# Kernel tuning notes

Hardware: AMD Instinct MI355X
Metric: run time of the kernel (lower is better)

## Reference

```python
import jax, jax.numpy as jnp
import numpy as np
from functools import partial

N = 50000
IN_C, HID_C, OUT_C = 256, 128, 64
E = 800000


def gcn_norm(src, dst, n_nodes):
    # PyG gcn_norm with unit edge weights: deg from target index, D^-1/2 A D^-1/2
    ones = jnp.ones(src.shape[0], dtype=jnp.float32)
    deg = jax.ops.segment_sum(ones, dst, num_segments=n_nodes)
    dinv = jnp.where(deg > 0, jax.lax.rsqrt(deg), 0.0)
    return dinv[src] * dinv[dst]


def gcn_conv(x, src, dst, norm, W, b):
    h = x @ W                              # [N, out] dense GEMM first (PyG order)
    msg = h[src] * norm[:, None]           # gather + scale  [E', out]
    out = jax.ops.segment_sum(msg, dst, num_segments=x.shape[0])
    return out + b


def setup_inputs() -> dict:
    key = jax.random.key(0)
    ks = jax.random.split(key, 6)
    x = jax.random.normal(ks[0], (N, IN_C), dtype=jnp.float32)
    edge_index = jax.random.randint(ks[1], (2, E), 0, N, dtype=jnp.int32)
    # Glorot-ish init for weights
    W1 = jax.random.normal(ks[2], (IN_C, HID_C), dtype=jnp.float32) / np.sqrt(IN_C)
    b1 = jnp.zeros((HID_C,), dtype=jnp.float32)
    W2 = jax.random.normal(ks[3], (HID_C, OUT_C), dtype=jnp.float32) / np.sqrt(HID_C)
    b2 = jnp.zeros((OUT_C,), dtype=jnp.float32)
    return {"x": x, "edge_index": edge_index, "W1": W1, "b1": b1, "W2": W2, "b2": b2}


def reference(x, edge_index, W1, b1, W2, b2):
    # eval mode: dropout is identity
    n = x.shape[0]
    loop = jnp.arange(n, dtype=edge_index.dtype)
    src = jnp.concatenate([edge_index[0], loop])   # add self loops (static E+N)
    dst = jnp.concatenate([edge_index[1], loop])
    norm = gcn_norm(src, dst, n)
    h = jax.nn.relu(gcn_conv(x, src, dst, norm, W1, b1))
    return gcn_conv(h, src, dst, norm, W2, b2)
```

## Files before the change

### kernel.cpp

```cpp
#include <hip/hip_runtime.h>


#define TPB 256
#define NBKT 196
#define P1_BLKS 98
#define PB_CAP 96
#define EB_CAP 4608
#define CSR_CAP 6400
#define P1_EPB 8192

typedef __bf16 bf16x8 __attribute__((ext_vector_type(8)));
typedef __bf16 bf16x4 __attribute__((ext_vector_type(4)));
typedef __bf16 bf16x2 __attribute__((ext_vector_type(2)));
typedef float f32x4 __attribute__((ext_vector_type(4)));

__device__ __forceinline__ float bflo(unsigned u) { return __uint_as_float(u << 16); }
__device__ __forceinline__ float bfhi(unsigned u) { return __uint_as_float(u & 0xffff0000u); }

__device__ __forceinline__ void gemm1_body(int bid, int tid, const float* __restrict__ x,
                                           const float* __restrict__ W1,
                                           __bf16* __restrict__ outp, int M) {
    int wave = tid >> 6, lane = tid & 63;
    int col = lane & 15, q = lane >> 4;
    long rb = (long)bid * 128 + wave * 32;
    long r0 = rb + col, r1 = rb + 16 + col;
    long r0c = (r0 < M) ? r0 : (M - 1);
    long r1c = (r1 < M) ? r1 : (M - 1);

    f32x4 acc[8][2];
#pragma unroll
    for (int o = 0; o < 8; o++) {
        acc[o][0] = (f32x4){0.f, 0.f, 0.f, 0.f};
        acc[o][1] = (f32x4){0.f, 0.f, 0.f, 0.f};
    }

#pragma unroll
    for (int ks = 0; ks < 8; ks++) {
        int k0 = ks * 32 + q * 8;
        const float* A0 = x + r0c * 256 + k0;
        const float* A1 = x + r1c * 256 + k0;
        float4 f0a = *(const float4*)A0;
        float4 f0b = *(const float4*)(A0 + 4);
        float4 f1a = *(const float4*)A1;
        float4 f1b = *(const float4*)(A1 + 4);
        bf16x8 b0, b1;
        b0[0] = (__bf16)f0a.x; b0[1] = (__bf16)f0a.y; b0[2] = (__bf16)f0a.z; b0[3] = (__bf16)f0a.w;
        b0[4] = (__bf16)f0b.x; b0[5] = (__bf16)f0b.y; b0[6] = (__bf16)f0b.z; b0[7] = (__bf16)f0b.w;
        b1[0] = (__bf16)f1a.x; b1[1] = (__bf16)f1a.y; b1[2] = (__bf16)f1a.z; b1[3] = (__bf16)f1a.w;
        b1[4] = (__bf16)f1b.x; b1[5] = (__bf16)f1b.y; b1[6] = (__bf16)f1b.z; b1[7] = (__bf16)f1b.w;
        const float* wp = W1 + (long)k0 * 128 + col;
#pragma unroll
        for (int ot = 0; ot < 8; ot++) {
            bf16x8 a;
#pragma unroll
            for (int j = 0; j < 8; j++) a[j] = (__bf16)wp[j * 128 + ot * 16];
            acc[ot][0] = __builtin_amdgcn_mfma_f32_16x16x32_bf16(a, b0, acc[ot][0], 0, 0, 0);
            acc[ot][1] = __builtin_amdgcn_mfma_f32_16x16x32_bf16(a, b1, acc[ot][1], 0, 0, 0);
        }
    }

#pragma unroll
    for (int ot = 0; ot < 8; ot++) {
        int oc = ot * 16 + q * 4;
        if (r0 < M) {
            bf16x4 v;
#pragma unroll
            for (int r = 0; r < 4; r++) v[r] = (__bf16)acc[ot][0][r];
            *(bf16x4*)(outp + r0 * 128 + oc) = v;
        }
        if (r1 < M) {
            bf16x4 v;
#pragma unroll
            for (int r = 0; r < 4; r++) v[r] = (__bf16)acc[ot][1][r];
            *(bf16x4*)(outp + r1 * 128 + oc) = v;
        }
    }
}

__global__ __launch_bounds__(256) void p1_gemm1_kernel(
    const int* __restrict__ src, const int* __restrict__ dst, int E, int p1Blocks,
    unsigned* __restrict__ gcnt2, unsigned* __restrict__ ebuf2,
    const float* __restrict__ x, const float* __restrict__ W1,
    __bf16* __restrict__ h1u, int M) {
    __shared__ int sCnt[256];
    int bx = (int)blockIdx.x, t = threadIdx.x;
    if (bx < p1Blocks) {
        sCnt[t] = 0;
        __syncthreads();
        long e0 = (long)bx * P1_EPB;
        int cnt = (int)(E - e0);
        if (cnt > P1_EPB) cnt = P1_EPB;
        unsigned* myslice = ebuf2 + (long)bx * NBKT * PB_CAP;
        for (int i = t; i < cnt; i += 256) {
            unsigned s = (unsigned)src[e0 + i];
            unsigned d = (unsigned)dst[e0 + i];
            int b = (int)(d >> 8);
            int pos = atomicAdd(&sCnt[b], 1);
            if (pos < PB_CAP) myslice[b * PB_CAP + pos] = (s << 16) | d;
        }
        __syncthreads();
        if (t < NBKT) {
            int c = sCnt[t];
            gcnt2[bx * NBKT + t] = (unsigned)(c < PB_CAP ? c : PB_CAP);
        }
    } else {
        gemm1_body(bx - p1Blocks, t, x, W1, h1u, M);
    }
}

__global__ __launch_bounds__(256) void csr_kernel(
    const unsigned* __restrict__ gcnt2, const unsigned* __restrict__ ebuf2,
    int* __restrict__ csr, int2* __restrict__ se, float* __restrict__ dinv,
    __bf16* __restrict__ h2s, int N) {
    __shared__ unsigned sEdges[EB_CAP];
    __shared__ int sCnt[256];
    __shared__ int sScan[256];
    __shared__ int sTot;
    int b = blockIdx.x, t = threadIdx.x;
    if (b == 0) {
        if (t == 0) dinv[N] = 0.0f;
        if (t < 32) ((unsigned*)(h2s + (long)N * 64))[t] = 0u;
    }
    sCnt[t] = 0;
    if (t == 0) sTot = 0;
    __syncthreads();
    if (t < P1_BLKS) {
        int c = (int)gcnt2[t * NBKT + b];
        int pos = atomicAdd(&sTot, c);
        const unsigned* chunk = ebuf2 + ((long)t * NBKT + b) * PB_CAP;
        for (int i = 0; i < c; i++) {
            if (pos + i >= EB_CAP) break;
            unsigned p = chunk[i];
            sEdges[pos + i] = p;
            atomicAdd(&sCnt[p & 255u], 1);
        }
    }
    __syncthreads();
    int m = sTot;
    if (m > EB_CAP) m = EB_CAP;
    int c = sCnt[t];
    int pad = (c + 7) & ~7;
    sScan[t] = pad;
    __syncthreads();
    for (int off = 1; off < 256; off <<= 1) {
        int v = (t >= off) ? sScan[t - off] : 0;
        __syncthreads();
        sScan[t] += v;
        __syncthreads();
    }
    int start = b * CSR_CAP + sScan[t] - pad;
    int node = (b << 8) + t;
    if (node < N) {
        se[node] = make_int2(start, start + pad);
        dinv[node] = rsqrtf((float)c + 1.0f);
    }
    __syncthreads();
    sCnt[t] = start;
    __syncthreads();
    for (int i = t; i < m; i += 256) {
        unsigned p = sEdges[i];
        int pos = atomicAdd(&sCnt[p & 255u], 1);
        csr[pos] = (int)(p >> 16);
    }
    if (node < N) {
        for (int k = start + c; k < start + pad; k++) csr[k] = N;
    }
}

#define ACC8()                                             \
    do {                                                   \
        a0x += bflo(v0) * w0; a0y += bfhi(v0) * w0;        \
        a1x += bflo(v1) * w1; a1y += bfhi(v1) * w1;        \
        a2x += bflo(v2) * w2; a2y += bfhi(v2) * w2;        \
        a3x += bflo(v3) * w3; a3y += bfhi(v3) * w3;        \
        a0x += bflo(v4) * w4; a0y += bfhi(v4) * w4;        \
        a1x += bflo(v5) * w5; a1y += bfhi(v5) * w5;        \
        a2x += bflo(v6) * w6; a2y += bfhi(v6) * w6;        \
        a3x += bflo(v7) * w7; a3y += bfhi(v7) * w7;        \
    } while (0)

__global__ __launch_bounds__(256) void agg128_gemm2_kernel(
    const __bf16* __restrict__ h, const int* __restrict__ csr,
    const int2* __restrict__ se, const float* __restrict__ dinv,
    const float* __restrict__ bias, const float* __restrict__ W2,
    __bf16* __restrict__ h2s, int N) {
    __shared__ __bf16 stash[16 * 132];
    int wave = threadIdx.x >> 6, lane = threadIdx.x & 63;
    int n0 = blockIdx.x * 16;
    unsigned* stw = (unsigned*)stash;

    float2 bv = ((const float2*)bias)[lane];
#pragma unroll 1
    for (int i = 0; i < 4; i++) {
        int n = n0 + wave * 4 + i;
        float ox = 0.f, oy = 0.f;
        if (n < N) {
            int2 s_e = se[n];
            int start = s_e.x, m = s_e.y - s_e.x;
            float dn = dinv[n];
            const unsigned* hp = (const unsigned*)h;
            const int* sl = csr + start;
            unsigned self = hp[(long)n * 64 + lane];
            float a0x = bflo(self) * dn, a0y = bfhi(self) * dn;
            float a1x = 0.f, a1y = 0.f, a2x = 0.f, a2y = 0.f, a3x = 0.f, a3y = 0.f;
            if (m > 0) {
                int4 c0 = *(const int4*)sl;
                int4 c1 = *(const int4*)(sl + 4);
                int i0 = __builtin_amdgcn_readfirstlane(c0.x);
                int i1 = __builtin_amdgcn_readfirstlane(c0.y);
                int i2 = __builtin_amdgcn_readfirstlane(c0.z);
                int i3 = __builtin_amdgcn_readfirstlane(c0.w);
                int i4 = __builtin_amdgcn_readfirstlane(c1.x);
                int i5 = __builtin_amdgcn_readfirstlane(c1.y);
                int i6 = __builtin_amdgcn_readfirstlane(c1.z);
                int i7 = __builtin_amdgcn_readfirstlane(c1.w);
                unsigned v0 = hp[(long)i0 * 64 + lane], v1 = hp[(long)i1 * 64 + lane];
                unsigned v2 = hp[(long)i2 * 64 + lane], v3 = hp[(long)i3 * 64 + lane];
                unsigned v4 = hp[(long)i4 * 64 + lane], v5 = hp[(long)i5 * 64 + lane];
                unsigned v6 = hp[(long)i6 * 64 + lane], v7 = hp[(long)i7 * 64 + lane];
                float w0 = dinv[i0], w1 = dinv[i1], w2 = dinv[i2], w3 = dinv[i3];
                float w4 = dinv[i4], w5 = dinv[i5], w6 = dinv[i6], w7 = dinv[i7];
                int4 d0 = *(const int4*)(sl + 8);
                int4 d1 = *(const int4*)(sl + 12);
                for (int j = 8; j < m; j += 8) {
                    int t0 = __builtin_amdgcn_readfirstlane(d0.x);
                    int t1 = __builtin_amdgcn_readfirstlane(d0.y);
                    int t2 = __builtin_amdgcn_readfirstlane(d0.z);
                    int t3 = __builtin_amdgcn_readfirstlane(d0.w);
                    int t4 = __builtin_amdgcn_readfirstlane(d1.x);
                    int t5 = __builtin_amdgcn_readfirstlane(d1.y);
                    int t6 = __builtin_amdgcn_readfirstlane(d1.z);
                    int t7 = __builtin_amdgcn_readfirstlane(d1.w);
                    unsigned u0 = hp[(long)t0 * 64 + lane], u1 = hp[(long)t1 * 64 + lane];
                    unsigned u2 = hp[(long)t2 * 64 + lane], u3 = hp[(long)t3 * 64 + lane];
                    unsigned u4 = hp[(long)t4 * 64 + lane], u5 = hp[(long)t5 * 64 + lane];
                    unsigned u6 = hp[(long)t6 * 64 + lane], u7 = hp[(long)t7 * 64 + lane];
                    float q0 = dinv[t0], q1 = dinv[t1], q2 = dinv[t2], q3 = dinv[t3];
                    float q4 = dinv[t4], q5 = dinv[t5], q6 = dinv[t6], q7 = dinv[t7];
                    d0 = *(const int4*)(sl + j + 8);
                    d1 = *(const int4*)(sl + j + 12);
                    ACC8();
                    v0 = u0; v1 = u1; v2 = u2; v3 = u3; v4 = u4; v5 = u5; v6 = u6; v7 = u7;
                    w0 = q0; w1 = q1; w2 = q2; w3 = q3; w4 = q4; w5 = q5; w6 = q6; w7 = q7;
                }
                ACC8();
            }
            ox = fmaxf((a0x + a1x + a2x + a3x) * dn + bv.x, 0.f);
            oy = fmaxf((a0y + a1y + a2y + a3y) * dn + bv.y, 0.f);
        }
        bf16x2 st = {(__bf16)ox, (__bf16)oy};
        stw[(wave * 4 + i) * 66 + lane] = *(unsigned*)&st;
    }
    __syncthreads();

    int col = lane & 15, q = lane >> 4;
    const __bf16* srow = stash + col * 132;
    f32x4 acc = (f32x4){0.f, 0.f, 0.f, 0.f};
#pragma unroll
    for (int ks = 0; ks < 4; ks++) {
        bf16x8 bb = *(const bf16x8*)(srow + ks * 32 + q * 8);
        const float* wp = W2 + (long)(ks * 32 + q * 8) * 64 + wave * 16 + col;
        bf16x8 a;
#pragma unroll
        for (int j = 0; j < 8; j++) a[j] = (__bf16)wp[j * 64];
        acc = __builtin_amdgcn_mfma_f32_16x16x32_bf16(a, bb, acc, 0, 0, 0);
    }
    int node = n0 + col;
    if (node < N) {
        float dn2 = dinv[node];
        bf16x4 v;
#pragma unroll
        for (int r = 0; r < 4; r++) v[r] = (__bf16)(acc[r] * dn2);
        *(bf16x4*)(h2s + (long)node * 64 + (wave * 16 + q * 4)) = v;
    }
}
#undef ACC8

#define ACC8B()                                                                            \
    do {                                                                                   \
        a0 += __uint_as_float((unsigned)v0 << 16); a1 += __uint_as_float((unsigned)v1 << 16); \
        a2 += __uint_as_float((unsigned)v2 << 16); a3 += __uint_as_float((unsigned)v3 << 16); \
        a0 += __uint_as_float((unsigned)v4 << 16); a1 += __uint_as_float((unsigned)v5 << 16); \
        a2 += __uint_as_float((unsigned)v6 << 16); a3 += __uint_as_float((unsigned)v7 << 16); \
    } while (0)

__global__ __launch_bounds__(256) void agg64_kernel(const __bf16* __restrict__ hs,
                                                    const int* __restrict__ csr,
                                                    const int2* __restrict__ se,
                                                    const float* __restrict__ dinv,
                                                    const float* __restrict__ bias,
                                                    float* __restrict__ outp, int N) {
    int gid = blockIdx.x * TPB + threadIdx.x;
    int n = gid >> 6, lane = gid & 63;
    if (n >= N) return;
    int2 s_e = se[n];
    int start = s_e.x, m = s_e.y - s_e.x;
    float dn = dinv[n];
    const unsigned short* hp = (const unsigned short*)hs;
    const int* sl = csr + start;
    float a0 = __uint_as_float(((unsigned)hp[(long)n * 64 + lane]) << 16);
    float a1 = 0.f, a2 = 0.f, a3 = 0.f;
    if (m > 0) {
        int4 c0 = *(const int4*)sl;
        int4 c1 = *(const int4*)(sl + 4);
        int i0 = __builtin_amdgcn_readfirstlane(c0.x);
        int i1 = __builtin_amdgcn_readfirstlane(c0.y);
        int i2 = __builtin_amdgcn_readfirstlane(c0.z);
        int i3 = __builtin_amdgcn_readfirstlane(c0.w);
        int i4 = __builtin_amdgcn_readfirstlane(c1.x);
        int i5 = __builtin_amdgcn_readfirstlane(c1.y);
        int i6 = __builtin_amdgcn_readfirstlane(c1.z);
        int i7 = __builtin_amdgcn_readfirstlane(c1.w);
        unsigned short v0 = hp[(long)i0 * 64 + lane], v1 = hp[(long)i1 * 64 + lane];
        unsigned short v2 = hp[(long)i2 * 64 + lane], v3 = hp[(long)i3 * 64 + lane];
        unsigned short v4 = hp[(long)i4 * 64 + lane], v5 = hp[(long)i5 * 64 + lane];
        unsigned short v6 = hp[(long)i6 * 64 + lane], v7 = hp[(long)i7 * 64 + lane];
        int4 d0 = *(const int4*)(sl + 8);
        int4 d1 = *(const int4*)(sl + 12);
        for (int j = 8; j < m; j += 8) {
            int t0 = __builtin_amdgcn_readfirstlane(d0.x);
            int t1 = __builtin_amdgcn_readfirstlane(d0.y);
            int t2 = __builtin_amdgcn_readfirstlane(d0.z);
            int t3 = __builtin_amdgcn_readfirstlane(d0.w);
            int t4 = __builtin_amdgcn_readfirstlane(d1.x);
            int t5 = __builtin_amdgcn_readfirstlane(d1.y);
            int t6 = __builtin_amdgcn_readfirstlane(d1.z);
            int t7 = __builtin_amdgcn_readfirstlane(d1.w);
            unsigned short u0 = hp[(long)t0 * 64 + lane], u1 = hp[(long)t1 * 64 + lane];
            unsigned short u2 = hp[(long)t2 * 64 + lane], u3 = hp[(long)t3 * 64 + lane];
            unsigned short u4 = hp[(long)t4 * 64 + lane], u5 = hp[(long)t5 * 64 + lane];
            unsigned short u6 = hp[(long)t6 * 64 + lane], u7 = hp[(long)t7 * 64 + lane];
            d0 = *(const int4*)(sl + j + 8);
            d1 = *(const int4*)(sl + j + 12);
            ACC8B();
            v0 = u0; v1 = u1; v2 = u2; v3 = u3; v4 = u4; v5 = u5; v6 = u6; v7 = u7;
        }
        ACC8B();
    }
    outp[(long)n * 64 + lane] = (a0 + a1 + a2 + a3) * dn + bias[lane];
}
#undef ACC8B

static inline int cdiv(long a, long b) { return (int)((a + b - 1) / b); }

extern "C" void kernel_launch(void* const* d_in, const int* in_sizes, int n_in,
                              void* d_out, int out_size, void* d_ws, size_t ws_size,
                              hipStream_t stream) {
    const float* x  = (const float*)d_in[0];
    const int*   ei = (const int*)d_in[1];
    const float* W1 = (const float*)d_in[2];
    const float* b1 = (const float*)d_in[3];
    const float* W2 = (const float*)d_in[4];
    const float* b2 = (const float*)d_in[5];

    const int IN_C = 256;
    const int N = in_sizes[0] / IN_C;
    const int E = in_sizes[1] / 2;
    const int* src = ei;
    const int* dst = ei + E;

    char* w = (char*)d_ws;
    size_t off = 0;
    auto alloc = [&](size_t bytes) { void* p = w + off; off = (off + bytes + 255) & ~255ull; return p; };
    __bf16*   h1u   = (__bf16*)alloc((size_t)(N + 1) * 128 * 2);
    __bf16*   h2s   = (__bf16*)alloc((size_t)(N + 1) * 64 * 2);
    unsigned* ebuf2 = (unsigned*)alloc((size_t)P1_BLKS * NBKT * PB_CAP * 4);
    int*      csr   = (int*)alloc((size_t)NBKT * CSR_CAP * 4);
    int2*     se    = (int2*)alloc((size_t)N * 8);
    float*    dinv  = (float*)alloc((size_t)(N + 1) * 4);
    unsigned* gcnt2 = (unsigned*)alloc((size_t)P1_BLKS * NBKT * 4);

    int p1Blocks = P1_BLKS;
    int gemmBlocks = cdiv(N, 128);
    p1_gemm1_kernel<<<p1Blocks + gemmBlocks, TPB, 0, stream>>>(
        src, dst, E, p1Blocks, gcnt2, ebuf2, x, W1, h1u, N);

    csr_kernel<<<NBKT, TPB, 0, stream>>>(gcnt2, ebuf2, csr, se, dinv, h2s, N);

    agg128_gemm2_kernel<<<cdiv(N, 16), TPB, 0, stream>>>(h1u, csr, se, dinv, b1,
                                                         W2, h2s, N);

    agg64_kernel<<<cdiv((long)N * 64, TPB), TPB, 0, stream>>>(h2s, csr, se, dinv, b2,
                                                              (float*)d_out, N);
}
```

Baseline: 193.2 us.

## Stage W1 fragments in LDS for GEMM1 and prepack W2 to bf16 once

GEMM1 now gives each block 64 rows (one 16-row tile per wave) instead of 128. It loads and converts its x rows to bf16 once, and builds each 16-column W1 fragment tile in shared memory so all four waves share it, where before every wave did strided fp32 gathers of W1. Extra blocks appended to the CSR kernel prepack W2 into MFMA-ready bf16x8 fragments, so the aggregation+GEMM2 kernel loads one vector per k-step instead of eight strided floats. The partition block count is also derived from E at runtime. The cost is more GEMM1 blocks, two barriers per output tile, and serialized W tile loads.

```diff
diff --git a/kernel.cpp b/kernel.cpp
--- a/kernel.cpp
+++ b/kernel.cpp
@@ -3,11 +3,10 @@
 
 #define TPB 256
 #define NBKT 196
-#define P1_BLKS 98
+#define P1_EPB 8192
 #define PB_CAP 96
 #define EB_CAP 4608
 #define CSR_CAP 6400
-#define P1_EPB 8192
 
 typedef __bf16 bf16x8 __attribute__((ext_vector_type(8)));
 typedef __bf16 bf16x4 __attribute__((ext_vector_type(4)));
@@ -16,66 +15,6 @@
 
 __device__ __forceinline__ float bflo(unsigned u) { return __uint_as_float(u << 16); }
 __device__ __forceinline__ float bfhi(unsigned u) { return __uint_as_float(u & 0xffff0000u); }
-
-__device__ __forceinline__ void gemm1_body(int bid, int tid, const float* __restrict__ x,
-                                           const float* __restrict__ W1,
-                                           __bf16* __restrict__ outp, int M) {
-    int wave = tid >> 6, lane = tid & 63;
-    int col = lane & 15, q = lane >> 4;
-    long rb = (long)bid * 128 + wave * 32;
-    long r0 = rb + col, r1 = rb + 16 + col;
-    long r0c = (r0 < M) ? r0 : (M - 1);
-    long r1c = (r1 < M) ? r1 : (M - 1);
-
-    f32x4 acc[8][2];
-#pragma unroll
-    for (int o = 0; o < 8; o++) {
-        acc[o][0] = (f32x4){0.f, 0.f, 0.f, 0.f};
-        acc[o][1] = (f32x4){0.f, 0.f, 0.f, 0.f};
-    }
-
-#pragma unroll
-    for (int ks = 0; ks < 8; ks++) {
-        int k0 = ks * 32 + q * 8;
-        const float* A0 = x + r0c * 256 + k0;
-        const float* A1 = x + r1c * 256 + k0;
-        float4 f0a = *(const float4*)A0;
-        float4 f0b = *(const float4*)(A0 + 4);
-        float4 f1a = *(const float4*)A1;
-        float4 f1b = *(const float4*)(A1 + 4);
-        bf16x8 b0, b1;
-        b0[0] = (__bf16)f0a.x; b0[1] = (__bf16)f0a.y; b0[2] = (__bf16)f0a.z; b0[3] = (__bf16)f0a.w;
-        b0[4] = (__bf16)f0b.x; b0[5] = (__bf16)f0b.y; b0[6] = (__bf16)f0b.z; b0[7] = (__bf16)f0b.w;
-        b1[0] = (__bf16)f1a.x; b1[1] = (__bf16)f1a.y; b1[2] = (__bf16)f1a.z; b1[3] = (__bf16)f1a.w;
-        b1[4] = (__bf16)f1b.x; b1[5] = (__bf16)f1b.y; b1[6] = (__bf16)f1b.z; b1[7] = (__bf16)f1b.w;
-        const float* wp = W1 + (long)k0 * 128 + col;
-#pragma unroll
-        for (int ot = 0; ot < 8; ot++) {
-            bf16x8 a;
-#pragma unroll
-            for (int j = 0; j < 8; j++) a[j] = (__bf16)wp[j * 128 + ot * 16];
-            acc[ot][0] = __builtin_amdgcn_mfma_f32_16x16x32_bf16(a, b0, acc[ot][0], 0, 0, 0);
-            acc[ot][1] = __builtin_amdgcn_mfma_f32_16x16x32_bf16(a, b1, acc[ot][1], 0, 0, 0);
-        }
-    }
-
-#pragma unroll
-    for (int ot = 0; ot < 8; ot++) {
-        int oc = ot * 16 + q * 4;
-        if (r0 < M) {
-            bf16x4 v;
-#pragma unroll
-            for (int r = 0; r < 4; r++) v[r] = (__bf16)acc[ot][0][r];
-            *(bf16x4*)(outp + r0 * 128 + oc) = v;
-        }
-        if (r1 < M) {
-            bf16x4 v;
-#pragma unroll
-            for (int r = 0; r < 4; r++) v[r] = (__bf16)acc[ot][1][r];
-            *(bf16x4*)(outp + r1 * 128 + oc) = v;
-        }
-    }
-}
 
 __global__ __launch_bounds__(256) void p1_gemm1_kernel(
     const int* __restrict__ src, const int* __restrict__ dst, int E, int p1Blocks,
@@ -83,6 +22,7 @@
     const float* __restrict__ x, const float* __restrict__ W1,
     __bf16* __restrict__ h1u, int M) {
     __shared__ int sCnt[256];
+    __shared__ bf16x8 wtile[8 * 64];
     int bx = (int)blockIdx.x, t = threadIdx.x;
     if (bx < p1Blocks) {
         sCnt[t] = 0;
@@ -103,20 +43,87 @@
             int c = sCnt[t];
             gcnt2[bx * NBKT + t] = (unsigned)(c < PB_CAP ? c : PB_CAP);
         }
-    } else {
-        gemm1_body(bx - p1Blocks, t, x, W1, h1u, M);
+        return;
+    }
+    int bid = bx - p1Blocks;
+    int lane = t & 63, wave = t >> 6;
+    int col = lane & 15, q = lane >> 4;
+    long r0 = (long)bid * 64 + wave * 16 + col;
+    long r0c = (r0 < M) ? r0 : (M - 1);
+
+    bf16x8 bvec[8];
+#pragma unroll
+    for (int ks = 0; ks < 8; ks++) {
+        int k0 = ks * 32 + q * 8;
+        const float* A0 = x + r0c * 256 + k0;
+        float4 f0a = *(const float4*)A0;
+        float4 f0b = *(const float4*)(A0 + 4);
+        bf16x8 b0;
+        b0[0] = (__bf16)f0a.x; b0[1] = (__bf16)f0a.y; b0[2] = (__bf16)f0a.z; b0[3] = (__bf16)f0a.w;
+        b0[4] = (__bf16)f0b.x; b0[5] = (__bf16)f0b.y; b0[6] = (__bf16)f0b.z; b0[7] = (__bf16)f0b.w;
+        bvec[ks] = b0;
+    }
+
+    f32x4 acc[8];
+#pragma unroll
+    for (int o = 0; o < 8; o++) acc[o] = (f32x4){0.f, 0.f, 0.f, 0.f};
+
+#pragma unroll 1
+    for (int ot = 0; ot < 8; ot++) {
+#pragma unroll
+        for (int s = t; s < 512; s += 256) {
+            int ksS = s >> 6, L = s & 63;
+            int c = ot * 16 + (L & 15);
+            int k0 = ksS * 32 + (L >> 4) * 8;
+            bf16x8 v;
+#pragma unroll
+            for (int j = 0; j < 8; j++) v[j] = (__bf16)W1[(k0 + j) * 128 + c];
+            wtile[s] = v;
+        }
+        __syncthreads();
+#pragma unroll
+        for (int ks = 0; ks < 8; ks++)
+            acc[ot] = __builtin_amdgcn_mfma_f32_16x16x32_bf16(wtile[ks * 64 + lane],
+                                                              bvec[ks], acc[ot], 0, 0, 0);
+        __syncthreads();
+    }
+
+    if (r0 < M) {
+#pragma unroll
+        for (int ot = 0; ot < 8; ot++) {
+            int oc = ot * 16 + q * 4;
+            bf16x4 v;
+#pragma unroll
+            for (int r = 0; r < 4; r++) v[r] = (__bf16)acc[ot][r];
+            *(bf16x4*)(h1u + r0 * 128 + oc) = v;
+        }
     }
 }
 
 __global__ __launch_bounds__(256) void csr_kernel(
     const unsigned* __restrict__ gcnt2, const unsigned* __restrict__ ebuf2,
     int* __restrict__ csr, int2* __restrict__ se, float* __restrict__ dinv,
-    __bf16* __restrict__ h2s, int N) {
+    __bf16* __restrict__ h2s, int N, int p1Blocks,
+    const float* __restrict__ W2, __bf16* __restrict__ wf2) {
     __shared__ unsigned sEdges[EB_CAP];
     __shared__ int sCnt[256];
     __shared__ int sScan[256];
     __shared__ int sTot;
     int b = blockIdx.x, t = threadIdx.x;
+    if (b >= NBKT) {
+        int g2 = (b - NBKT) * 256 + t;
+        if (g2 < 16 * 64) {
+            int frag = g2 >> 6, L = g2 & 63;
+            int kstep = frag >> 2, oct = frag & 3;
+            int oc = oct * 16 + (L & 15);
+            int k0 = kstep * 32 + (L >> 4) * 8;
+            bf16x8 v;
+#pragma unroll
+            for (int j = 0; j < 8; j++) v[j] = (__bf16)W2[(k0 + j) * 64 + oc];
+            ((bf16x8*)wf2)[g2] = v;
+        }
+        return;
+    }
     if (b == 0) {
         if (t == 0) dinv[N] = 0.0f;
         if (t < 32) ((unsigned*)(h2s + (long)N * 64))[t] = 0u;
@@ -124,7 +131,7 @@
     sCnt[t] = 0;
     if (t == 0) sTot = 0;
     __syncthreads();
-    if (t < P1_BLKS) {
+    if (t < p1Blocks) {
         int c = (int)gcnt2[t * NBKT + b];
         int pos = atomicAdd(&sTot, c);
         const unsigned* chunk = ebuf2 + ((long)t * NBKT + b) * PB_CAP;
@@ -182,7 +189,7 @@
 __global__ __launch_bounds__(256) void agg128_gemm2_kernel(
     const __bf16* __restrict__ h, const int* __restrict__ csr,
     const int2* __restrict__ se, const float* __restrict__ dinv,
-    const float* __restrict__ bias, const float* __restrict__ W2,
+    const float* __restrict__ bias, const bf16x8* __restrict__ wf2,
     __bf16* __restrict__ h2s, int N) {
     __shared__ __bf16 stash[16 * 132];
     int wave = threadIdx.x >> 6, lane = threadIdx.x & 63;
@@ -259,10 +266,7 @@
 #pragma unroll
     for (int ks = 0; ks < 4; ks++) {
         bf16x8 bb = *(const bf16x8*)(srow + ks * 32 + q * 8);
-        const float* wp = W2 + (long)(ks * 32 + q * 8) * 64 + wave * 16 + col;
-        bf16x8 a;
-#pragma unroll
-        for (int j = 0; j < 8; j++) a[j] = (__bf16)wp[j * 64];
+        bf16x8 a = wf2[(ks * 4 + wave) * 64 + lane];
         acc = __builtin_amdgcn_mfma_f32_16x16x32_bf16(a, bb, acc, 0, 0, 0);
     }
     int node = n0 + col;
@@ -362,23 +366,25 @@
     char* w = (char*)d_ws;
     size_t off = 0;
     auto alloc = [&](size_t bytes) { void* p = w + off; off = (off + bytes + 255) & ~255ull; return p; };
+    int p1Blocks = cdiv(E, P1_EPB);
     __bf16*   h1u   = (__bf16*)alloc((size_t)(N + 1) * 128 * 2);
     __bf16*   h2s   = (__bf16*)alloc((size_t)(N + 1) * 64 * 2);
-    unsigned* ebuf2 = (unsigned*)alloc((size_t)P1_BLKS * NBKT * PB_CAP * 4);
+    unsigned* ebuf2 = (unsigned*)alloc((size_t)p1Blocks * NBKT * PB_CAP * 4);
     int*      csr   = (int*)alloc((size_t)NBKT * CSR_CAP * 4);
     int2*     se    = (int2*)alloc((size_t)N * 8);
     float*    dinv  = (float*)alloc((size_t)(N + 1) * 4);
-    unsigned* gcnt2 = (unsigned*)alloc((size_t)P1_BLKS * NBKT * 4);
-
-    int p1Blocks = P1_BLKS;
-    int gemmBlocks = cdiv(N, 128);
+    unsigned* gcnt2 = (unsigned*)alloc((size_t)p1Blocks * NBKT * 4);
+    __bf16*   wf2   = (__bf16*)alloc(16 * 64 * 8 * 2);
+
+    int gemmBlocks = cdiv(N, 64);
     p1_gemm1_kernel<<<p1Blocks + gemmBlocks, TPB, 0, stream>>>(
         src, dst, E, p1Blocks, gcnt2, ebuf2, x, W1, h1u, N);
 
-    csr_kernel<<<NBKT, TPB, 0, stream>>>(gcnt2, ebuf2, csr, se, dinv, h2s, N);
+    csr_kernel<<<NBKT + 4, TPB, 0, stream>>>(gcnt2, ebuf2, csr, se, dinv, h2s, N,
+                                             p1Blocks, W2, wf2);
 
     agg128_gemm2_kernel<<<cdiv(N, 16), TPB, 0, stream>>>(h1u, csr, se, dinv, b1,
-                                                         W2, h2s, N);
+                                                         (const bf16x8*)wf2, h2s, N);
 
     agg64_kernel<<<cdiv((long)N * 64, TPB), TPB, 0, stream>>>(h2s, csr, se, dinv, b2,
                                                               (float*)d_out, N);
```

After: 188.9 us. 2.2% less time.
